# Kernel tuning notes

Measured on AMD Instinct MI355X. Metric: run time of the kernel, lower is better.

Reference implementation:

```python
import jax, jax.numpy as jnp
import numpy as np

N = 4096
INP_DIM = 256
EMB_DIM = 256
ALPHA = 0.01  # LeakyReLU negative slope
NEG_INF = -9.0e15


def _xavier(key, shape, gain=1.414):
    fan_in, fan_out = shape[0], shape[1]
    limit = gain * np.sqrt(6.0 / (fan_in + fan_out))
    return jax.random.uniform(key, shape, jnp.float32, -limit, limit)


def setup_inputs() -> dict:
    key = jax.random.key(0)
    ks = jax.random.split(key, 9)
    inp = {
        "input": jax.random.normal(ks[0], (N, INP_DIM), jnp.float32),
        "adj": jax.random.randint(ks[1], (N, N), 0, 2, jnp.int32),
        "W0": _xavier(ks[2], (INP_DIM, EMB_DIM)),
        "W1": _xavier(ks[3], (EMB_DIM, EMB_DIM)),
        "a1": _xavier(ks[4], (2 * EMB_DIM, 1)),
        "W2": _xavier(ks[5], (EMB_DIM, EMB_DIM)),
        "a2": _xavier(ks[6], (2 * EMB_DIM, 1)),
        "W3": _xavier(ks[7], (EMB_DIM, EMB_DIM)),
        "a3": _xavier(ks[8], (2 * EMB_DIM, 1)),
    }
    return inp


def _gat_layer(h, adj, W, a):
    # h: [N, F_in], W: [F_in, F], a: [2F, 1]
    Wh = h @ W                       # [N, F]
    F_out = Wh.shape[1]
    # e_ij = leakyrelu([Wh_i || Wh_j] @ a) = leakyrelu(Wh_i@a1 + Wh_j@a2)
    f1 = Wh @ a[:F_out]              # [N, 1]
    f2 = Wh @ a[F_out:]              # [N, 1]
    e = jax.nn.leaky_relu(f1 + f2.T, ALPHA)            # [N, N]
    att = jnp.where(adj > 0, e, NEG_INF)
    att = jax.nn.softmax(att, axis=1)                    # masked softmax over neighbors
    h_prime = att @ Wh                                   # [N, F]
    return jax.nn.elu(h_prime)                           # concat=True -> ELU


def reference(input, adj, W0, W1, a1, W2, a2, W3, a3):
    h = input @ W0                   # GAT-level projection
    h = _gat_layer(h, adj, W1, a1)
    h = _gat_layer(h, adj, W2, a2)
    h = _gat_layer(h, adj, W3, a3)
    return h
```

## Files before the change

kernel.cpp:

```cpp
#include <hip/hip_runtime.h>
#include <hip/hip_bf16.h>
#include <cstdint>
#include <cstddef>

#define NN 4096
#define FD 256
#define WPR 64

typedef __attribute__((ext_vector_type(8))) unsigned short ushort8v;
typedef __attribute__((ext_vector_type(4))) unsigned short ushort4v;
typedef __attribute__((ext_vector_type(8))) short short8;
typedef __attribute__((ext_vector_type(4))) float float4v;

#define C1 30.0f
#define C2 0.3f

static __device__ __forceinline__ unsigned short f2bf(float x) {
    union { float f; unsigned int u; } v; v.f = x;
    unsigned int r = v.u + 0x7FFFu + ((v.u >> 16) & 1u);
    return (unsigned short)(r >> 16);
}

static __device__ __forceinline__ short8 as_s8(ushort8v v) {
    union { ushort8v u; short8 s; } x; x.u = v; return x.s;
}

__global__ __launch_bounds__(256) void setup(const int* __restrict__ adj,
                                             const float* __restrict__ input,
                                             const float* __restrict__ W0, const float* __restrict__ W1,
                                             const float* __restrict__ W2, const float* __restrict__ W3,
                                             unsigned long long* __restrict__ bits,
                                             unsigned short* __restrict__ hb,
                                             unsigned short* __restrict__ Wbt,
                                             float* __restrict__ f1f2) {
    const int b = blockIdx.x;
    const int t = threadIdx.x;
    if (b < 4096) {
        const int wave = t >> 6, lane = t & 63;
        const int* arow = adj + (size_t)b * NN;
        #pragma unroll
        for (int it = 0; it < NN / 256; ++it) {
            int j = it * 256 + wave * 64 + lane;
            unsigned long long m = __ballot(arow[j] > 0);
            if (lane == 0) bits[(size_t)b * WPR + (it * 4 + wave)] = m;
        }
        hb[(size_t)b * 256 + t] = f2bf(input[(size_t)b * 256 + t]);
    } else if (b < 5120) {
        int idx = (b - 4096) * 256 + t;
        int mat = idx >> 16;
        int within = idx & 65535;
        int n = within >> 8, k = within & 255;
        const float* W = (mat == 0) ? W0 : (mat == 1) ? W1 : (mat == 2) ? W2 : W3;
        Wbt[idx] = f2bf(W[k * 256 + n]);
    } else {
        #pragma unroll
        for (int i = 0; i < 24; ++i) {
            int pos = i * 1024 + (b - 5120) * 256 + t;
            f1f2[pos] = 0.f;
        }
    }
}

__global__ __launch_bounds__(256) void proj_gemm(const unsigned short* __restrict__ A,
                                                 const unsigned short* __restrict__ Bt,
                                                 const float* __restrict__ av,
                                                 float* __restrict__ f1f2,
                                                 unsigned short* __restrict__ Cbt,
                                                 unsigned short* __restrict__ Crow) {
    const int t = threadIdx.x;
    const int bm = blockIdx.x >> 2, bn = blockIdx.x & 3;
    const int m0 = bm * 64, n0 = bn * 64;
    __shared__ unsigned short As[64 * 264];
    __shared__ unsigned short Bs[64 * 264];
    const int lane = t & 63, wave = t >> 6;
    const int wm = (wave >> 1) * 32, wn = (wave & 1) * 32;
    const int lr = t >> 2, lc0 = (t & 3) * 8;
    #pragma unroll
    for (int i = 0; i < 8; ++i) {
        int col = lc0 + i * 32;
        *(ushort8v*)&As[lr * 264 + col] = *(const ushort8v*)&A[(size_t)(m0 + lr) * 256 + col];
        *(ushort8v*)&Bs[lr * 264 + col] = *(const ushort8v*)&Bt[(size_t)(n0 + lr) * 256 + col];
    }
    __syncthreads();
    float4v acc[2][2] = {{{0.f,0.f,0.f,0.f},{0.f,0.f,0.f,0.f}},{{0.f,0.f,0.f,0.f},{0.f,0.f,0.f,0.f}}};
    #pragma unroll
    for (int kk = 0; kk < 256; kk += 32) {
        const int kc = kk + (lane >> 4) * 8;
        #pragma unroll
        for (int fm = 0; fm < 2; ++fm) {
            short8 a = as_s8(*(const ushort8v*)&As[(wm + fm * 16 + (lane & 15)) * 264 + kc]);
            #pragma unroll
            for (int fn = 0; fn < 2; ++fn) {
                short8 b = as_s8(*(const ushort8v*)&Bs[(wn + fn * 16 + (lane & 15)) * 264 + kc]);
                acc[fm][fn] = __builtin_amdgcn_mfma_f32_16x16x32_bf16(a, b, acc[fm][fn], 0, 0, 0);
            }
        }
    }

    const int rb = wm + (lane >> 4) * 4;
    const int cb = wn + (lane & 15);
    if (Crow) {
        #pragma unroll
        for (int fm = 0; fm < 2; ++fm)
            #pragma unroll
            for (int fn = 0; fn < 2; ++fn)
                #pragma unroll
                for (int r = 0; r < 4; ++r)
                    Crow[(size_t)(m0 + rb + fm * 16 + r) * 256 + n0 + cb + fn * 16] = f2bf(acc[fm][fn][r]);
    }

    if (f1f2) {
        float a1c[2], a2c[2];
        #pragma unroll
        for (int fn = 0; fn < 2; ++fn) {
            a1c[fn] = av[n0 + cb + fn * 16];
            a2c[fn] = av[256 + n0 + cb + fn * 16];
        }
        #pragma unroll
        for (int fm = 0; fm < 2; ++fm)
            #pragma unroll
            for (int r = 0; r < 4; ++r) {
                float s1 = acc[fm][0][r] * a1c[0] + acc[fm][1][r] * a1c[1];
                float s2 = acc[fm][0][r] * a2c[0] + acc[fm][1][r] * a2c[1];
                #pragma unroll
                for (int off = 1; off < 16; off <<= 1) {
                    s1 += __shfl_xor(s1, off, 64);
                    s2 += __shfl_xor(s2, off, 64);
                }
                if ((lane & 15) == 0) {
                    int row = m0 + rb + fm * 16 + r;
                    atomicAdd(&f1f2[row], s1);
                    atomicAdd(&f1f2[4096 + row], s2);
                }
            }
    }

    if (Cbt) {
        unsigned short* T = As;
        __syncthreads();
        #pragma unroll
        for (int fm = 0; fm < 2; ++fm)
            #pragma unroll
            for (int fn = 0; fn < 2; ++fn)
                #pragma unroll
                for (int r = 0; r < 4; ++r)
                    T[(cb + fn * 16) * 72 + rb + fm * 16 + r] = f2bf(acc[fm][fn][r]);
        __syncthreads();
        const int tr = t >> 2;
        #pragma unroll
        for (int i = 0; i < 2; ++i) {
            int tc = (t & 3) * 8 + i * 32;
            *(ushort8v*)&Cbt[(size_t)(n0 + tr) * 4096 + m0 + tc] = *(const ushort8v*)&T[tr * 72 + tc];
        }
    }
}

__global__ __launch_bounds__(256) void rowcoef(const unsigned long long* __restrict__ bits,
                                               const float* __restrict__ f1f2,
                                               float4* __restrict__ rowco,
                                               float2* __restrict__ tab2g) {
    __shared__ float2 tl[4096];
    const int t = threadIdx.x;
    const float* f2p = f1f2 + 4096;
    #pragma unroll
    for (int i = 0; i < 16; ++i) {
        float v = f2p[i * 256 + t];
        float2 pr = make_float2(__expf(v - C1), __expf(0.01f * v - C2));
        tl[i * 256 + t] = pr;
        if (blockIdx.x == 0) tab2g[i * 256 + t] = pr;
    }
    __syncthreads();
    const int lane = t & 63, wave = t >> 6;
    for (int rr = 0; rr < 2; ++rr) {
        const int row = blockIdx.x * 8 + wave * 2 + rr;
        const unsigned long long wl = bits[(size_t)row * WPR + lane];
        const float f1r = f1f2[row];
        const float th = __expf(-f1r - C1);
        float mx = 0.f, S1 = 0.f, S2 = 0.f;
        #pragma unroll 16
        for (int b = 0; b < 64; ++b) {
            unsigned long long w = __shfl(wl, b, 64);
            bool bit = (w >> lane) & 1ULL;
            float2 v = tl[b * 64 + lane];
            float ebm = bit ? v.x : 0.f;
            mx = fmaxf(mx, ebm);
            bool cond = v.x > th;
            S1 += (bit && cond)  ? v.x : 0.f;
            S2 += (bit && !cond) ? v.y : 0.f;
        }
        #pragma unroll
        for (int off = 1; off < 64; off <<= 1) {
            mx = fmaxf(mx, __shfl_xor(mx, off, 64));
            S1 += __shfl_xor(S1, off, 64);
            S2 += __shfl_xor(S2, off, 64);
        }
        if (lane == 0) {
            float M  = C1 + __logf(mx);
            float fm_ = f1r + M;
            float m  = fm_ > 0.f ? fm_ : 0.01f * fm_;
            float alpha = __expf(fminf(f1r + C1 - m, 60.f));
            float gamma = __expf(fminf(0.01f * (f1r + C1) - m, 60.f));
            float inv = 1.0f / (alpha * S1 + gamma * S2);
            rowco[row] = make_float4(alpha * inv, gamma * inv, th, 0.f);
        }
    }
}

__global__ __launch_bounds__(256, 2) void att_flat(const unsigned long long* __restrict__ bits,
                                                   const float4* __restrict__ rowco,
                                                   const float2* __restrict__ tab2,
                                                   const unsigned short* __restrict__ Bt,
                                                   float* __restrict__ part, int kchunk) {
    const int t = threadIdx.x;
    const int bm = blockIdx.x & 63;
    const int ks = blockIdx.x >> 6;
    const int m0 = bm * 64;
    const int k0 = ks * kchunk;
    const int lane = t & 63, wave = t >> 6;
    const int wn = wave * 64;
    const int g = lane >> 4, ml = lane & 15;

    float pA[4], pG[4], thE[4];
    #pragma unroll
    for (int fm = 0; fm < 4; ++fm) {
        float4 rc = rowco[m0 + fm * 16 + ml];
        pA[fm] = rc.x; pG[fm] = rc.y; thE[fm] = rc.z;
    }
    const unsigned long long* bitb = bits + (size_t)(m0 + ml) * WPR;
    const unsigned short* bbase = Bt + (size_t)(wn + ml) * 4096 + g * 8;

    float4v acc[4][4];
    #pragma unroll
    for (int i = 0; i < 4; ++i)
        #pragma unroll
        for (int j = 0; j < 4; ++j) acc[i][j] = (float4v){0.f, 0.f, 0.f, 0.f};

    for (int kk = k0; kk < k0 + kchunk; kk += 64) {
        const int word = kk >> 6;
        unsigned long long w64[4];
        #pragma unroll
        for (int fm = 0; fm < 4; ++fm) w64[fm] = bitb[(size_t)(fm * 16) * WPR + word];
        ushort8v breg[4][2];
        #pragma unroll
        for (int fn = 0; fn < 4; ++fn)
            #pragma unroll
            for (int h = 0; h < 2; ++h)
                breg[fn][h] = *(const ushort8v*)&bbase[(size_t)(fn * 16) * 4096 + kk + h * 32];

        #pragma unroll
        for (int h = 0; h < 2; ++h) {
            float tb[8], td[8];
            const float4v* q = (const float4v*)&tab2[kk + h * 32 + g * 8];
            #pragma unroll
            for (int i = 0; i < 4; ++i) {
                float4v v = q[i];
                tb[2 * i] = v[0]; td[2 * i] = v[1]; tb[2 * i + 1] = v[2]; td[2 * i + 1] = v[3];
            }
            short8 afr[4];
            #pragma unroll
            for (int fm = 0; fm < 4; ++fm) {
                unsigned int wh = (unsigned int)(w64[fm] >> (h * 32 + g * 8));
                ushort8v af;
                #pragma unroll
                for (int jj = 0; jj < 4; ++jj) {
                    float e0 = tb[2 * jj], e1 = tb[2 * jj + 1];
                    float p0 = ((wh >> (2 * jj)) & 1u)     ? (e0 > thE[fm] ? pA[fm] * e0 : pG[fm] * td[2 * jj])     : 0.f;
                    float p1 = ((wh >> (2 * jj + 1)) & 1u) ? (e1 > thE[fm] ? pA[fm] * e1 : pG[fm] * td[2 * jj + 1]) : 0.f;
                    union { __hip_bfloat162 b2; unsigned short us[2]; } cv;
                    cv.b2 = __float22bfloat162_rn(make_float2(p0, p1));
                    af[2 * jj] = cv.us[0]; af[2 * jj + 1] = cv.us[1];
                }
                afr[fm] = as_s8(af);
            }
            #pragma unroll
            for (int fm = 0; fm < 4; ++fm)
                #pragma unroll
                for (int fn = 0; fn < 4; ++fn)
                    acc[fm][fn] = __builtin_amdgcn_mfma_f32_16x16x32_bf16(afr[fm], as_s8(breg[fn][h]), acc[fm][fn], 0, 0, 0);
        }
    }

    const int rb = g * 4;
    const int cb = wn + ml;
    float* pbase = part + ((size_t)ks << 20);
    #pragma unroll
    for (int fm = 0; fm < 4; ++fm)
        #pragma unroll
        for (int fn = 0; fn < 4; ++fn)
            #pragma unroll
            for (int r = 0; r < 4; ++r)
                pbase[(size_t)(m0 + rb + fm * 16 + r) * 256 + cb + fn * 16] = acc[fm][fn][r];
}

__global__ __launch_bounds__(256) void att_reduce(const float* __restrict__ part,
                                                  float* __restrict__ outf,
                                                  unsigned short* __restrict__ hrow, int nsplit) {
    const int idx = (blockIdx.x * 256 + threadIdx.x) * 4;
    float4v s = *(const float4v*)&part[idx];
    for (int sp = 1; sp < nsplit; ++sp)
        s += *(const float4v*)&part[((size_t)sp << 20) + idx];
    float4v v;
    ushort4v hb;
    #pragma unroll
    for (int j = 0; j < 4; ++j) {
        float x = s[j];
        x = x > 0.f ? x : (__expf(x) - 1.f);
        v[j] = x;
        hb[j] = f2bf(x);
    }
    if (outf) *(float4v*)&outf[idx] = v;
    *(ushort4v*)&hrow[idx] = hb;
}

extern "C" void kernel_launch(void* const* d_in, const int* in_sizes, int n_in,
                              void* d_out, int out_size, void* d_ws, size_t ws_size,
                              hipStream_t stream) {
    const float* input = (const float*)d_in[0];
    const int*   adj   = (const int*)d_in[1];
    const float* W0    = (const float*)d_in[2];
    const float* W1    = (const float*)d_in[3];
    const float* a1    = (const float*)d_in[4];
    const float* W2    = (const float*)d_in[5];
    const float* a2    = (const float*)d_in[6];
    const float* W3    = (const float*)d_in[7];
    const float* a3    = (const float*)d_in[8];
    float* out = (float*)d_out;
    char* ws = (char*)d_ws;

    unsigned long long* bits = (unsigned long long*)(ws);
    unsigned short* h0   = (unsigned short*)(ws + (2u << 20));
    unsigned short* h1   = (unsigned short*)(ws + (4u << 20));
    unsigned short* Whbt = (unsigned short*)(ws + (6u << 20));
    unsigned short* Wbt  = (unsigned short*)(ws + (8u << 20));
    float*  f1f2  = (float*)(ws + (9u << 20));
    float4* rowco = (float4*)(ws + (10u << 20));
    float2* tab2  = (float2*)(ws + (10u << 20) + (256u << 10));
    float*  part  = (float*)(ws + (13u << 20));

    const size_t base = 13u << 20;
    int SPLIT = 8;
    while (SPLIT > 1 && base + (size_t)SPLIT * (4u << 20) > ws_size) SPLIT >>= 1;
    const int kchunk = NN / SPLIT;

    float* f1f2_l[3] = { f1f2, f1f2 + 8192, f1f2 + 16384 };

    setup<<<5124, 256, 0, stream>>>(adj, input, W0, W1, W2, W3, bits, h0, Wbt, f1f2);

    proj_gemm<<<256, 256, 0, stream>>>(h0, Wbt + 0 * 65536, nullptr, nullptr, nullptr, h1);

    proj_gemm<<<256, 256, 0, stream>>>(h1, Wbt + 1 * 65536, a1, f1f2_l[0], Whbt, nullptr);
    rowcoef<<<512, 256, 0, stream>>>(bits, f1f2_l[0], rowco, tab2);
    att_flat<<<64 * SPLIT, 256, 0, stream>>>(bits, rowco, tab2, Whbt, part, kchunk);
    att_reduce<<<1024, 256, 0, stream>>>(part, nullptr, h0, SPLIT);

    proj_gemm<<<256, 256, 0, stream>>>(h0, Wbt + 2 * 65536, a2, f1f2_l[1], Whbt, nullptr);
    rowcoef<<<512, 256, 0, stream>>>(bits, f1f2_l[1], rowco, tab2);
    att_flat<<<64 * SPLIT, 256, 0, stream>>>(bits, rowco, tab2, Whbt, part, kchunk);
    att_reduce<<<1024, 256, 0, stream>>>(part, nullptr, h1, SPLIT);

    proj_gemm<<<256, 256, 0, stream>>>(h1, Wbt + 3 * 65536, a3, f1f2_l[2], Whbt, nullptr);
    rowcoef<<<512, 256, 0, stream>>>(bits, f1f2_l[2], rowco, tab2);
    att_flat<<<64 * SPLIT, 256, 0, stream>>>(bits, rowco, tab2, Whbt, part, kchunk);
    att_reduce<<<1024, 256, 0, stream>>>(part, out, h0, SPLIT);
}
```

Measured before the change: 329.6 us.

## Restructure attention GEMM into 128x128 LDS-staged tiles with shared probability generation

The attention-times-features kernel moves from 64-row blocks covering all 256 output columns, with every wave recomputing the full A fragment in registers, to 128x128 output tiles. Each thread now builds one 16-element slice of the masked softmax probabilities and copies a B slice into padded shared memory, and all waves read their fragments from there. This is meant to remove the redundant per-wave probability computation and raise reuse of the A and B operands. In exchange each 32-wide k step adds two barriers, does no double buffering, and computes each probability twice across the two column halves.

```diff
diff --git a/kernel.cpp b/kernel.cpp
--- a/kernel.cpp
+++ b/kernel.cpp
@@ -206,28 +206,28 @@
     }
 }
 
-__global__ __launch_bounds__(256, 2) void att_flat(const unsigned long long* __restrict__ bits,
+__global__ __launch_bounds__(256, 2) void att_gemm(const unsigned long long* __restrict__ bits,
                                                    const float4* __restrict__ rowco,
                                                    const float2* __restrict__ tab2,
                                                    const unsigned short* __restrict__ Bt,
                                                    float* __restrict__ part, int kchunk) {
     const int t = threadIdx.x;
-    const int bm = blockIdx.x & 63;
+    const int bm = blockIdx.x & 31;
+    const int bn = (blockIdx.x >> 5) & 1;
     const int ks = blockIdx.x >> 6;
-    const int m0 = bm * 64;
+    const int m0 = bm * 128, n0 = bn * 128;
     const int k0 = ks * kchunk;
+    __shared__ unsigned short As[128 * 40];
+    __shared__ unsigned short Bs[128 * 40];
     const int lane = t & 63, wave = t >> 6;
-    const int wn = wave * 64;
+    const int wm = (wave >> 1) * 64, wn = (wave & 1) * 64;
     const int g = lane >> 4, ml = lane & 15;
-
-    float pA[4], pG[4], thE[4];
-    #pragma unroll
-    for (int fm = 0; fm < 4; ++fm) {
-        float4 rc = rowco[m0 + fm * 16 + ml];
-        pA[fm] = rc.x; pG[fm] = rc.y; thE[fm] = rc.z;
-    }
-    const unsigned long long* bitb = bits + (size_t)(m0 + ml) * WPR;
-    const unsigned short* bbase = Bt + (size_t)(wn + ml) * 4096 + g * 8;
+    const int r = t >> 1, kh = (t & 1) * 16;
+
+    const float4 rc = rowco[m0 + r];
+    const float pA = rc.x, pG = rc.y, th = rc.z;
+    const unsigned long long* brow = bits + (size_t)(m0 + r) * WPR;
+    const unsigned short* bsrc = Bt + (size_t)(n0 + r) * 4096 + kh;
 
     float4v acc[4][4];
     #pragma unroll
@@ -235,61 +235,51 @@
         #pragma unroll
         for (int j = 0; j < 4; ++j) acc[i][j] = (float4v){0.f, 0.f, 0.f, 0.f};
 
-    for (int kk = k0; kk < k0 + kchunk; kk += 64) {
-        const int word = kk >> 6;
-        unsigned long long w64[4];
-        #pragma unroll
-        for (int fm = 0; fm < 4; ++fm) w64[fm] = bitb[(size_t)(fm * 16) * WPR + word];
-        ushort8v breg[4][2];
+    for (int kk = k0; kk < k0 + kchunk; kk += 32) {
+        ushort8v b0 = *(const ushort8v*)&bsrc[kk];
+        ushort8v b1 = *(const ushort8v*)&bsrc[kk + 8];
+        unsigned int wb = (unsigned int)((brow[kk >> 6] >> ((kk & 63) + kh)) & 0xFFFFu);
+        const float4v* q = (const float4v*)&tab2[kk + kh];
+        ushort8v p0, p1;
+        #pragma unroll
+        for (int jj = 0; jj < 8; ++jj) {
+            float4v v = q[jj];
+            float x0 = ((wb >> (2 * jj)) & 1u)     ? (v[0] > th ? pA * v[0] : pG * v[1]) : 0.f;
+            float x1 = ((wb >> (2 * jj + 1)) & 1u) ? (v[2] > th ? pA * v[2] : pG * v[3]) : 0.f;
+            union { __hip_bfloat162 b2; unsigned int u; } cv;
+            cv.b2 = __float22bfloat162_rn(make_float2(x0, x1));
+            if (jj < 4) ((unsigned int*)&p0)[jj] = cv.u;
+            else        ((unsigned int*)&p1)[jj - 4] = cv.u;
+        }
+        *(ushort8v*)&As[r * 40 + kh]     = p0;
+        *(ushort8v*)&As[r * 40 + kh + 8] = p1;
+        *(ushort8v*)&Bs[r * 40 + kh]     = b0;
+        *(ushort8v*)&Bs[r * 40 + kh + 8] = b1;
+        __syncthreads();
+        const int kc = g * 8;
+        short8 a[4], b[4];
+        #pragma unroll
+        for (int fm = 0; fm < 4; ++fm)
+            a[fm] = as_s8(*(const ushort8v*)&As[(wm + fm * 16 + ml) * 40 + kc]);
         #pragma unroll
         for (int fn = 0; fn < 4; ++fn)
-            #pragma unroll
-            for (int h = 0; h < 2; ++h)
-                breg[fn][h] = *(const ushort8v*)&bbase[(size_t)(fn * 16) * 4096 + kk + h * 32];
-
-        #pragma unroll
-        for (int h = 0; h < 2; ++h) {
-            float tb[8], td[8];
-            const float4v* q = (const float4v*)&tab2[kk + h * 32 + g * 8];
-            #pragma unroll
-            for (int i = 0; i < 4; ++i) {
-                float4v v = q[i];
-                tb[2 * i] = v[0]; td[2 * i] = v[1]; tb[2 * i + 1] = v[2]; td[2 * i + 1] = v[3];
-            }
-            short8 afr[4];
-            #pragma unroll
-            for (int fm = 0; fm < 4; ++fm) {
-                unsigned int wh = (unsigned int)(w64[fm] >> (h * 32 + g * 8));
-                ushort8v af;
-                #pragma unroll
-                for (int jj = 0; jj < 4; ++jj) {
-                    float e0 = tb[2 * jj], e1 = tb[2 * jj + 1];
-                    float p0 = ((wh >> (2 * jj)) & 1u)     ? (e0 > thE[fm] ? pA[fm] * e0 : pG[fm] * td[2 * jj])     : 0.f;
-                    float p1 = ((wh >> (2 * jj + 1)) & 1u) ? (e1 > thE[fm] ? pA[fm] * e1 : pG[fm] * td[2 * jj + 1]) : 0.f;
-                    union { __hip_bfloat162 b2; unsigned short us[2]; } cv;
-                    cv.b2 = __float22bfloat162_rn(make_float2(p0, p1));
-                    af[2 * jj] = cv.us[0]; af[2 * jj + 1] = cv.us[1];
-                }
-                afr[fm] = as_s8(af);
-            }
-            #pragma unroll
-            for (int fm = 0; fm < 4; ++fm)
-                #pragma unroll
-                for (int fn = 0; fn < 4; ++fn)
-                    acc[fm][fn] = __builtin_amdgcn_mfma_f32_16x16x32_bf16(afr[fm], as_s8(breg[fn][h]), acc[fm][fn], 0, 0, 0);
-        }
-    }
-
-    const int rb = g * 4;
-    const int cb = wn + ml;
+            b[fn] = as_s8(*(const ushort8v*)&Bs[(wn + fn * 16 + ml) * 40 + kc]);
+        #pragma unroll
+        for (int fm = 0; fm < 4; ++fm)
+            #pragma unroll
+            for (int fn = 0; fn < 4; ++fn)
+                acc[fm][fn] = __builtin_amdgcn_mfma_f32_16x16x32_bf16(a[fm], b[fn], acc[fm][fn], 0, 0, 0);
+        __syncthreads();
+    }
+
     float* pbase = part + ((size_t)ks << 20);
     #pragma unroll
     for (int fm = 0; fm < 4; ++fm)
         #pragma unroll
         for (int fn = 0; fn < 4; ++fn)
             #pragma unroll
-            for (int r = 0; r < 4; ++r)
-                pbase[(size_t)(m0 + rb + fm * 16 + r) * 256 + cb + fn * 16] = acc[fm][fn][r];
+            for (int rr = 0; rr < 4; ++rr)
+                pbase[(size_t)(m0 + wm + fm * 16 + g * 4 + rr) * 256 + n0 + wn + fn * 16 + ml] = acc[fm][fn][rr];
 }
 
 __global__ __launch_bounds__(256) void att_reduce(const float* __restrict__ part,
@@ -350,16 +340,16 @@
 
     proj_gemm<<<256, 256, 0, stream>>>(h1, Wbt + 1 * 65536, a1, f1f2_l[0], Whbt, nullptr);
     rowcoef<<<512, 256, 0, stream>>>(bits, f1f2_l[0], rowco, tab2);
-    att_flat<<<64 * SPLIT, 256, 0, stream>>>(bits, rowco, tab2, Whbt, part, kchunk);
+    att_gemm<<<64 * SPLIT, 256, 0, stream>>>(bits, rowco, tab2, Whbt, part, kchunk);
     att_reduce<<<1024, 256, 0, stream>>>(part, nullptr, h0, SPLIT);
 
     proj_gemm<<<256, 256, 0, stream>>>(h0, Wbt + 2 * 65536, a2, f1f2_l[1], Whbt, nullptr);
     rowcoef<<<512, 256, 0, stream>>>(bits, f1f2_l[1], rowco, tab2);
-    att_flat<<<64 * SPLIT, 256, 0, stream>>>(bits, rowco, tab2, Whbt, part, kchunk);
+    att_gemm<<<64 * SPLIT, 256, 0, stream>>>(bits, rowco, tab2, Whbt, part, kchunk);
     att_reduce<<<1024, 256, 0, stream>>>(part, nullptr, h1, SPLIT);
 
     proj_gemm<<<256, 256, 0, stream>>>(h1, Wbt + 3 * 65536, a3, f1f2_l[2], Whbt, nullptr);
     rowcoef<<<512, 256, 0, stream>>>(bits, f1f2_l[2], rowco, tab2);
-    att_flat<<<64 * SPLIT, 256, 0, stream>>>(bits, rowco, tab2, Whbt, part, kchunk);
+    att_gemm<<<64 * SPLIT, 256, 0, stream>>>(bits, rowco, tab2, Whbt, part, kchunk);
     att_reduce<<<1024, 256, 0, stream>>>(part, out, h0, SPLIT);
 }
```

Measured after the change: 328.4 us. About the same (-0.4%).
